# Optimization experiments

Measured on AMD Instinct MI355X. Metric: run time of the kernel, lower is better.

Reference implementation:

```python
import jax, jax.numpy as jnp
import numpy as np

SCALING = 2.0  # alpha / r = 128 / 64


def setup_inputs() -> dict:
    key = jax.random.key(0)
    k1, k2, k3, k4, k5 = jax.random.split(key, 5)
    B, S, DIN, DOUT, R = 4, 2048, 4096, 4096, 64
    x = jax.random.normal(k1, (B, S, DIN), dtype=jnp.float32)
    # int8 quantized weight codes in [-127, 127] (stored as int32 for portability)
    qweight = jax.random.randint(k2, (DOUT, DIN), -127, 128, dtype=jnp.int32)
    # per-output-row absmax dequant scale (already divided by 127)
    scale = jax.random.uniform(k3, (DOUT, 1), dtype=jnp.float32, minval=0.005, maxval=0.02)
    lora_A = jax.random.normal(k4, (R, DIN), dtype=jnp.float32) * 0.02
    lora_B = jax.random.normal(k5, (DOUT, R), dtype=jnp.float32) * 0.02
    return {"x": x, "qweight": qweight, "scale": scale, "lora_A": lora_A, "lora_B": lora_B}


def reference(x, qweight, scale, lora_A, lora_B):
    # inline int8 dequant: w[o,i] = code[o,i] * scale[o]
    w = qweight.astype(x.dtype) * scale  # [DOUT, DIN]
    base = jnp.einsum('bsi,oi->bso', x, w)
    # low-rank LoRA path: (x @ A^T) @ B^T, scaled
    xa = jnp.einsum('bsi,ri->bsr', x, lora_A)       # [B,S,R]
    lora = jnp.einsum('bsr,or->bso', xa, lora_B)    # [B,S,DOUT]
    return base + SCALING * lora
```

## Files before the change

### kernel.cpp

```cpp
#include <hip/hip_runtime.h>
#include <hip/hip_bf16.h>
#include <stdint.h>


typedef __bf16 bf16x8 __attribute__((ext_vector_type(8)));
typedef float f32x4 __attribute__((ext_vector_type(4)));
typedef int i32x4 __attribute__((ext_vector_type(4)));

#define DIN   4096
#define DOUT  4096
#define MTOT  8192
#define RNK   64
#define NT    64

__device__ inline void gload_lds16(const void* g, void* l) {
  __builtin_amdgcn_global_load_lds((const __attribute__((address_space(1))) void*)g,
                                   (__attribute__((address_space(3))) void*)l,
                                   16, 0, 0);
}

__global__ __launch_bounds__(256) void quant_x_kernel(const float* __restrict__ x,
                                                      signed char* __restrict__ Xi8,
                                                      float* __restrict__ tstep) {
  const int row = blockIdx.x, t = threadIdx.x;
  const float4* xr = (const float4*)(x + (size_t)row * DIN);
  float4 v[4];
  float m = 0.f;
#pragma unroll
  for (int s = 0; s < 4; ++s) {
    v[s] = xr[t + s * 256];
    m = fmaxf(m, fmaxf(fmaxf(fabsf(v[s].x), fabsf(v[s].y)),
                       fmaxf(fabsf(v[s].z), fabsf(v[s].w))));
  }
#pragma unroll
  for (int off = 32; off > 0; off >>= 1) m = fmaxf(m, __shfl_xor(m, off));
  __shared__ float wm[4];
  if ((t & 63) == 0) wm[t >> 6] = m;
  __syncthreads();
  m = fmaxf(fmaxf(wm[0], wm[1]), fmaxf(wm[2], wm[3]));
  m = fmaxf(m, 1e-30f);
  const float rs = 127.0f / m;
  int* orow = (int*)(Xi8 + (size_t)row * DIN);
#pragma unroll
  for (int s = 0; s < 4; ++s) {
    float e[4] = {v[s].x, v[s].y, v[s].z, v[s].w};
    union { signed char c[4]; int i; } p;
#pragma unroll
    for (int j = 0; j < 4; ++j) {
      int q = __float2int_rn(e[j] * rs);
      q = q > 127 ? 127 : (q < -127 ? -127 : q);
      p.c[j] = (signed char)q;
    }
    orow[t + s * 256] = p.i;
  }
  if (t == 0) tstep[row] = m * (1.0f / 127.0f);
}

__global__ void cvt_w_kernel(const int* __restrict__ q, signed char* __restrict__ Wi8) {
  int i = blockIdx.x * blockDim.x + threadIdx.x;
  int4 v = ((const int4*)q)[i];
  union { signed char c[4]; int i; } p;
  p.c[0] = (signed char)v.x; p.c[1] = (signed char)v.y;
  p.c[2] = (signed char)v.z; p.c[3] = (signed char)v.w;
  ((int*)Wi8)[i] = p.i;
}

__global__ __launch_bounds__(256) void cvt_ab_kernel(const float* __restrict__ A,
                                                     const float* __restrict__ B,
                                                     signed char* __restrict__ Ai8,
                                                     float* __restrict__ astep,
                                                     __bf16* __restrict__ Blt) {
  const int t = threadIdx.x;
  if (blockIdx.x < 64) {
    const int row = blockIdx.x;
    const float4* ar = (const float4*)(A + (size_t)row * DIN);
    float4 v[4];
    float m = 0.f;
#pragma unroll
    for (int s = 0; s < 4; ++s) {
      v[s] = ar[t + s * 256];
      m = fmaxf(m, fmaxf(fmaxf(fabsf(v[s].x), fabsf(v[s].y)),
                         fmaxf(fabsf(v[s].z), fabsf(v[s].w))));
    }
#pragma unroll
    for (int off = 32; off > 0; off >>= 1) m = fmaxf(m, __shfl_xor(m, off));
    __shared__ float wm[4];
    if ((t & 63) == 0) wm[t >> 6] = m;
    __syncthreads();
    m = fmaxf(fmaxf(wm[0], wm[1]), fmaxf(wm[2], wm[3]));
    m = fmaxf(m, 1e-30f);
    const float rs = 127.0f / m;
    int* orow = (int*)(Ai8 + (size_t)row * DIN);
#pragma unroll
    for (int s = 0; s < 4; ++s) {
      float e[4] = {v[s].x, v[s].y, v[s].z, v[s].w};
      union { signed char c[4]; int i; } p;
#pragma unroll
      for (int j = 0; j < 4; ++j) {
        int q = __float2int_rn(e[j] * rs);
        q = q > 127 ? 127 : (q < -127 ? -127 : q);
        p.c[j] = (signed char)q;
      }
      orow[t + s * 256] = p.i;
    }
    if (t == 0) astep[row] = m * (1.0f / 127.0f);
  } else {
    int i = (blockIdx.x - 64) * 256 + t;
    float4 v = ((const float4*)B)[i];
    union { __bf16 h[4]; uint64_t u; } p;
    p.h[0] = (__bf16)(2.0f * v.x); p.h[1] = (__bf16)(2.0f * v.y);
    p.h[2] = (__bf16)(2.0f * v.z); p.h[3] = (__bf16)(2.0f * v.w);
    ((uint64_t*)Blt)[i] = p.u;
  }
}

__global__ __launch_bounds__(128) void lora_xa_kernel(const signed char* __restrict__ Xi8,
                                                      const float* __restrict__ tstep,
                                                      const signed char* __restrict__ Ai8,
                                                      const float* __restrict__ astep,
                                                      __bf16* __restrict__ xa) {
  int wid = threadIdx.x >> 6, lane = threadIdx.x & 63;
  int rowbase = blockIdx.x * 32 + wid * 16;
  i32x4 acc[4] = {};
  const signed char* xrow = Xi8 + (size_t)(rowbase + (lane & 15)) * DIN + (lane >> 4) * 16;
  const signed char* ab = Ai8 + (size_t)(lane & 15) * DIN + (lane >> 4) * 16;
  for (int k0 = 0; k0 < DIN; k0 += 64) {
    i32x4 af = *(const i32x4*)(xrow + k0);
#pragma unroll
    for (int ni = 0; ni < 4; ++ni) {
      i32x4 bv = *(const i32x4*)(ab + (size_t)ni * 16 * DIN + k0);
      acc[ni] = __builtin_amdgcn_mfma_i32_16x16x64_i8(af, bv, acc[ni], 0, 0, 0);
    }
  }
  f32x4 tm = *(const f32x4*)&tstep[rowbase + (lane >> 4) * 4];
#pragma unroll
  for (int ni = 0; ni < 4; ++ni) {
    const int col = ni * 16 + (lane & 15);
    const float as = astep[col];
#pragma unroll
    for (int j = 0; j < 4; ++j) {
      int row = rowbase + (lane >> 4) * 4 + j;
      xa[(size_t)row * RNK + col] = (__bf16)((float)acc[ni][j] * tm[j] * as);
    }
  }
}

__global__ __launch_bounds__(512, 1) void gemm_i8_kernel(const signed char* __restrict__ Xi8,
                                                         const signed char* __restrict__ Wi8,
                                                         const float* __restrict__ scale,
                                                         const float* __restrict__ tstep,
                                                         const __bf16* __restrict__ xa,
                                                         const __bf16* __restrict__ Blt,
                                                         float* __restrict__ out) {
  extern __shared__ char smem[];
  const int tid = threadIdx.x;
  const int lane = tid & 63;
  const int w = tid >> 6;
  const int wr = w >> 2;
  const int wc = w & 3;

  const int swz = (blockIdx.x & 7) * 64 + (blockIdx.x >> 3);
  const int bx = swz & 15;
  const int by = swz >> 4;
  const size_t bm = (size_t)by * 256, bn = (size_t)bx * 256;

  const int rc = ((lane >> 4) ^ ((lane >> 1) & 3)) << 4;
  const int srow = tid >> 2;
  const int scol = ((tid & 3) ^ ((tid >> 3) & 3)) << 4;

  auto SH = [&](const signed char* g, size_t r0, int srct, int ldsoff) {
    gload_lds16(g + (r0 + srow) * (size_t)4096 + srct * 64 + scol,
                smem + ldsoff + tid * 16);
  };
  auto stage = [&](int srct, int buf) {
    int b = buf * 32768;
    SH(Xi8, bm, srct, b); SH(Xi8, bm + 128, srct, b + 8192);
    SH(Wi8, bn, srct, b + 16384); SH(Wi8, bn + 128, srct, b + 24576);
  };

  i32x4 aP[4], bP[4], aQ[4], bQ[4], a2[4];
  i32x4 acc[8][4] = {};

  stage(0, 0); stage(1, 1); stage(2, 2);
  asm volatile("s_waitcnt vmcnt(4)" ::: "memory");
  __builtin_amdgcn_s_barrier();
  {
    const int ab0 = wr * 8192 + (lane & 15) * 64 + rc;
    const int bb0 = 16384 + (wc >> 1) * 8192 + (wc & 1) * 4096 + (lane & 15) * 64 + rc;
#pragma unroll
    for (int mi = 0; mi < 4; ++mi) aP[mi] = *(const i32x4*)(smem + ab0 + mi * 1024);
#pragma unroll
    for (int ni = 0; ni < 4; ++ni) bP[ni] = *(const i32x4*)(smem + bb0 + ni * 1024);
  }

  auto body = [&](int kt, auto& ac, auto& bc, auto& an, auto& bn) {
    const int bufb = (kt & 3) * 32768;
    const int ab = bufb + wr * 8192 + (lane & 15) * 64 + rc;
    const int bb = bufb + 16384 + (wc >> 1) * 8192 + (wc & 1) * 4096 + (lane & 15) * 64 + rc;
    const int st = (kt + 3 < NT) ? kt + 3 : NT - 1;
    stage(st, (kt + 3) & 3);
#pragma unroll
    for (int mi = 0; mi < 4; ++mi)
      a2[mi] = *(const i32x4*)(smem + ab + 4096 + mi * 1024);
    __builtin_amdgcn_s_setprio(1);
#pragma unroll
    for (int mi = 0; mi < 4; ++mi)
#pragma unroll
      for (int ni = 0; ni < 4; ++ni)
        acc[mi][ni] = __builtin_amdgcn_mfma_i32_16x16x64_i8(ac[mi], bc[ni], acc[mi][ni], 0, 0, 0);
    __builtin_amdgcn_s_setprio(0);
    const int nbufb = ((kt + 1) & 3) * 32768;
    const int nab = nbufb + wr * 8192 + (lane & 15) * 64 + rc;
    const int nbb = nbufb + 16384 + (wc >> 1) * 8192 + (wc & 1) * 4096 + (lane & 15) * 64 + rc;
#pragma unroll
    for (int mi = 0; mi < 4; ++mi) an[mi] = *(const i32x4*)(smem + nab + mi * 1024);
#pragma unroll
    for (int ni = 0; ni < 4; ++ni) bn[ni] = *(const i32x4*)(smem + nbb + ni * 1024);
    __builtin_amdgcn_s_setprio(1);
#pragma unroll
    for (int mi = 0; mi < 4; ++mi)
#pragma unroll
      for (int ni = 0; ni < 4; ++ni)
        acc[4 + mi][ni] = __builtin_amdgcn_mfma_i32_16x16x64_i8(a2[mi], bc[ni], acc[4 + mi][ni], 0, 0, 0);
    __builtin_amdgcn_s_setprio(0);
    __builtin_amdgcn_sched_barrier(0);
    asm volatile("s_waitcnt vmcnt(4)" ::: "memory");
    __builtin_amdgcn_s_barrier();
  };

  for (int kt = 0; kt < NT; kt += 2) {
    body(kt, aP, bP, aQ, bQ);
    body(kt + 1, aQ, bQ, aP, bP);
  }

  const int sl_row = lane >> 3;
  const int sl_col = ((lane & 7) ^ (lane >> 3)) << 4;
  auto SBF = [&](const __bf16* g, size_t r0, int ldsoff) {
    char* d0 = smem + ldsoff + w * 2048 + lane * 16;
#pragma unroll
    for (int s = 0; s < 2; ++s) {
      const int rl = (w * 2 + s) * 8 + sl_row;
      gload_lds16((const char*)g + (r0 + rl) * 128 + sl_col, d0 + s * 1024);
    }
  };
  SBF(xa, bm, 0); SBF(xa, bm + 128, 16384);
  SBF(Blt, bn, 32768); SBF(Blt, bn + 128, 49152);

  float sc[4];
#pragma unroll
  for (int ni = 0; ni < 4; ++ni)
    sc[ni] = scale[bn + wc * 64 + ni * 16 + (lane & 15)];
  f32x4 tm[8];
#pragma unroll
  for (int mi = 0; mi < 8; ++mi)
    tm[mi] = *(const f32x4*)&tstep[bm + wr * 128 + mi * 16 + (lane >> 4) * 4];

  asm volatile("s_waitcnt vmcnt(0)" ::: "memory");
  __builtin_amdgcn_s_barrier();

  const int cx0 = ((lane >> 4) << 4) ^ ((lane & 7) << 4);
  const int cx1 = (64 | ((lane >> 4) << 4)) ^ ((lane & 7) << 4);
  const int abE = wr * 16384 + (lane & 15) * 128;
  const int bbE = 32768 + (wc >> 1) * 16384 + ((wc & 1) * 64 + (lane & 15)) * 128;

  bf16x8 bl0[4], bl1[4];
#pragma unroll
  for (int ni = 0; ni < 4; ++ni) {
    bl0[ni] = *(const bf16x8*)(smem + bbE + ni * 2048 + cx0);
    bl1[ni] = *(const bf16x8*)(smem + bbE + ni * 2048 + cx1);
  }
#pragma unroll
  for (int mi = 0; mi < 8; ++mi) {
    bf16x8 ax0 = *(const bf16x8*)(smem + abE + mi * 2048 + cx0);
    bf16x8 ax1 = *(const bf16x8*)(smem + abE + mi * 2048 + cx1);
    const size_t row = bm + wr * 128 + mi * 16 + (lane >> 4) * 4;
#pragma unroll
    for (int ni = 0; ni < 4; ++ni) {
      f32x4 l = {0.f, 0.f, 0.f, 0.f};
      l = __builtin_amdgcn_mfma_f32_16x16x32_bf16(ax0, bl0[ni], l, 0, 0, 0);
      l = __builtin_amdgcn_mfma_f32_16x16x32_bf16(ax1, bl1[ni], l, 0, 0, 0);
      const size_t col = bn + wc * 64 + ni * 16 + (lane & 15);
#pragma unroll
      for (int j = 0; j < 4; ++j)
        out[(row + j) * DOUT + col] = (float)acc[mi][ni][j] * (sc[ni] * tm[mi][j]) + l[j];
    }
  }
}

extern "C" void kernel_launch(void* const* d_in, const int* in_sizes, int n_in,
                              void* d_out, int out_size, void* d_ws, size_t ws_size,
                              hipStream_t stream) {
  const float* x = (const float*)d_in[0];
  const int* qw = (const int*)d_in[1];
  const float* scale = (const float*)d_in[2];
  const float* lA = (const float*)d_in[3];
  const float* lB = (const float*)d_in[4];
  float* out = (float*)d_out;

  char* ws = (char*)d_ws;
  signed char* Xi8 = (signed char*)ws;
  signed char* Wi8 = (signed char*)(ws + 33554432);
  __bf16* xa    = (__bf16*)(ws + 50331648);
  signed char* Ai8 = (signed char*)(ws + 51380224);
  __bf16* Blt   = (__bf16*)(ws + 51904512);
  float* tstep  = (float*)(ws + 52428800);
  float* astep  = (float*)(ws + 52461568);

  hipFuncSetAttribute((const void*)gemm_i8_kernel,
                      hipFuncAttributeMaxDynamicSharedMemorySize, 131072);

  quant_x_kernel<<<MTOT, 256, 0, stream>>>(x, Xi8, tstep);
  cvt_w_kernel<<<DOUT * (DIN / 4) / 256, 256, 0, stream>>>(qw, Wi8);
  cvt_ab_kernel<<<320, 256, 0, stream>>>(lA, lB, Ai8, astep, Blt);
  lora_xa_kernel<<<MTOT / 32, 128, 0, stream>>>(Xi8, tstep, Ai8, astep, xa);
  gemm_i8_kernel<<<(MTOT / 256) * (DOUT / 256), 512, 131072, stream>>>(
      Xi8, Wi8, scale, tstep, xa, Blt, out);
}
```

Baseline: 212.2 us.

## Merge prep kernels, split LoRA xa reduction over K, drop MFMA setprio

Three preprocessing kernels (x quantization, weight int32-to-int8 conversion, LoRA A/B conversion) are combined into one launch that picks its role from the block index. This removes launch gaps and tail serialization between them. The LoRA x·A^T kernel now splits K across four waves per 16-row block and reduces their results through shared memory, which gives more parallelism and shorter per-wave loops. The s_setprio hints around the main GEMM's MFMA blocks are removed, which changes wave scheduling in the hot loop and could help or hurt.

```diff
diff --git a/kernel.cpp b/kernel.cpp
--- a/kernel.cpp
+++ b/kernel.cpp
@@ -19,66 +19,30 @@
                                    16, 0, 0);
 }
 
-__global__ __launch_bounds__(256) void quant_x_kernel(const float* __restrict__ x,
-                                                      signed char* __restrict__ Xi8,
-                                                      float* __restrict__ tstep) {
-  const int row = blockIdx.x, t = threadIdx.x;
-  const float4* xr = (const float4*)(x + (size_t)row * DIN);
-  float4 v[4];
-  float m = 0.f;
-#pragma unroll
-  for (int s = 0; s < 4; ++s) {
-    v[s] = xr[t + s * 256];
-    m = fmaxf(m, fmaxf(fmaxf(fabsf(v[s].x), fabsf(v[s].y)),
-                       fmaxf(fabsf(v[s].z), fabsf(v[s].w))));
-  }
-#pragma unroll
-  for (int off = 32; off > 0; off >>= 1) m = fmaxf(m, __shfl_xor(m, off));
-  __shared__ float wm[4];
-  if ((t & 63) == 0) wm[t >> 6] = m;
-  __syncthreads();
-  m = fmaxf(fmaxf(wm[0], wm[1]), fmaxf(wm[2], wm[3]));
-  m = fmaxf(m, 1e-30f);
-  const float rs = 127.0f / m;
-  int* orow = (int*)(Xi8 + (size_t)row * DIN);
-#pragma unroll
-  for (int s = 0; s < 4; ++s) {
-    float e[4] = {v[s].x, v[s].y, v[s].z, v[s].w};
-    union { signed char c[4]; int i; } p;
-#pragma unroll
-    for (int j = 0; j < 4; ++j) {
-      int q = __float2int_rn(e[j] * rs);
-      q = q > 127 ? 127 : (q < -127 ? -127 : q);
-      p.c[j] = (signed char)q;
-    }
-    orow[t + s * 256] = p.i;
-  }
-  if (t == 0) tstep[row] = m * (1.0f / 127.0f);
-}
-
-__global__ void cvt_w_kernel(const int* __restrict__ q, signed char* __restrict__ Wi8) {
-  int i = blockIdx.x * blockDim.x + threadIdx.x;
-  int4 v = ((const int4*)q)[i];
-  union { signed char c[4]; int i; } p;
-  p.c[0] = (signed char)v.x; p.c[1] = (signed char)v.y;
-  p.c[2] = (signed char)v.z; p.c[3] = (signed char)v.w;
-  ((int*)Wi8)[i] = p.i;
-}
-
-__global__ __launch_bounds__(256) void cvt_ab_kernel(const float* __restrict__ A,
-                                                     const float* __restrict__ B,
-                                                     signed char* __restrict__ Ai8,
-                                                     float* __restrict__ astep,
-                                                     __bf16* __restrict__ Blt) {
-  const int t = threadIdx.x;
-  if (blockIdx.x < 64) {
-    const int row = blockIdx.x;
-    const float4* ar = (const float4*)(A + (size_t)row * DIN);
+__global__ __launch_bounds__(256) void prep_kernel(const float* __restrict__ x,
+                                                   const int* __restrict__ qw,
+                                                   const float* __restrict__ lA,
+                                                   const float* __restrict__ lB,
+                                                   signed char* __restrict__ Xi8,
+                                                   float* __restrict__ tstep,
+                                                   signed char* __restrict__ Wi8,
+                                                   signed char* __restrict__ Ai8,
+                                                   float* __restrict__ astep,
+                                                   __bf16* __restrict__ Blt) {
+  const int bid = blockIdx.x, t = threadIdx.x;
+  const float* src = nullptr;
+  signed char* dst = nullptr;
+  float* stp = nullptr;
+  int row = 0;
+  if (bid < 8192) { src = x; dst = Xi8; stp = tstep; row = bid; }
+  else if (bid < 8256) { src = lA; dst = Ai8; stp = astep; row = bid - 8192; }
+  if (src) {
+    const float4* xr = (const float4*)(src + (size_t)row * DIN);
     float4 v[4];
     float m = 0.f;
 #pragma unroll
     for (int s = 0; s < 4; ++s) {
-      v[s] = ar[t + s * 256];
+      v[s] = xr[t + s * 256];
       m = fmaxf(m, fmaxf(fmaxf(fabsf(v[s].x), fabsf(v[s].y)),
                          fmaxf(fabsf(v[s].z), fabsf(v[s].w))));
     }
@@ -90,7 +54,7 @@
     m = fmaxf(fmaxf(wm[0], wm[1]), fmaxf(wm[2], wm[3]));
     m = fmaxf(m, 1e-30f);
     const float rs = 127.0f / m;
-    int* orow = (int*)(Ai8 + (size_t)row * DIN);
+    int* orow = (int*)(dst + (size_t)row * DIN);
 #pragma unroll
     for (int s = 0; s < 4; ++s) {
       float e[4] = {v[s].x, v[s].y, v[s].z, v[s].w};
@@ -103,44 +67,62 @@
       }
       orow[t + s * 256] = p.i;
     }
-    if (t == 0) astep[row] = m * (1.0f / 127.0f);
-  } else {
-    int i = (blockIdx.x - 64) * 256 + t;
-    float4 v = ((const float4*)B)[i];
+    if (t == 0) stp[row] = m * (1.0f / 127.0f);
+  } else if (bid < 8512) {
+    int i = (bid - 8256) * 256 + t;
+    float4 v = ((const float4*)lB)[i];
     union { __bf16 h[4]; uint64_t u; } p;
     p.h[0] = (__bf16)(2.0f * v.x); p.h[1] = (__bf16)(2.0f * v.y);
     p.h[2] = (__bf16)(2.0f * v.z); p.h[3] = (__bf16)(2.0f * v.w);
     ((uint64_t*)Blt)[i] = p.u;
-  }
-}
-
-__global__ __launch_bounds__(128) void lora_xa_kernel(const signed char* __restrict__ Xi8,
+  } else {
+    int i = (bid - 8512) * 256 + t;
+    int4 v = ((const int4*)qw)[i];
+    union { signed char c[4]; int i; } p;
+    p.c[0] = (signed char)v.x; p.c[1] = (signed char)v.y;
+    p.c[2] = (signed char)v.z; p.c[3] = (signed char)v.w;
+    ((int*)Wi8)[i] = p.i;
+  }
+}
+
+__global__ __launch_bounds__(256) void lora_xa_kernel(const signed char* __restrict__ Xi8,
                                                       const float* __restrict__ tstep,
                                                       const signed char* __restrict__ Ai8,
                                                       const float* __restrict__ astep,
                                                       __bf16* __restrict__ xa) {
-  int wid = threadIdx.x >> 6, lane = threadIdx.x & 63;
-  int rowbase = blockIdx.x * 32 + wid * 16;
+  __shared__ i32x4 red[4][64][4];
+  const int w = threadIdx.x >> 6, lane = threadIdx.x & 63;
+  const int rowbase = blockIdx.x * 16;
   i32x4 acc[4] = {};
-  const signed char* xrow = Xi8 + (size_t)(rowbase + (lane & 15)) * DIN + (lane >> 4) * 16;
-  const signed char* ab = Ai8 + (size_t)(lane & 15) * DIN + (lane >> 4) * 16;
-  for (int k0 = 0; k0 < DIN; k0 += 64) {
-    i32x4 af = *(const i32x4*)(xrow + k0);
+  const int k00 = w * 1024 + (lane >> 4) * 16;
+  const signed char* xrow = Xi8 + (size_t)(rowbase + (lane & 15)) * DIN + k00;
+  const signed char* ab = Ai8 + (size_t)(lane & 15) * DIN + k00;
+#pragma unroll 4
+  for (int k = 0; k < 1024; k += 64) {
+    i32x4 af = *(const i32x4*)(xrow + k);
 #pragma unroll
     for (int ni = 0; ni < 4; ++ni) {
-      i32x4 bv = *(const i32x4*)(ab + (size_t)ni * 16 * DIN + k0);
+      i32x4 bv = *(const i32x4*)(ab + (size_t)ni * 16 * DIN + k);
       acc[ni] = __builtin_amdgcn_mfma_i32_16x16x64_i8(af, bv, acc[ni], 0, 0, 0);
     }
   }
-  f32x4 tm = *(const f32x4*)&tstep[rowbase + (lane >> 4) * 4];
-#pragma unroll
-  for (int ni = 0; ni < 4; ++ni) {
-    const int col = ni * 16 + (lane & 15);
-    const float as = astep[col];
-#pragma unroll
-    for (int j = 0; j < 4; ++j) {
-      int row = rowbase + (lane >> 4) * 4 + j;
-      xa[(size_t)row * RNK + col] = (__bf16)((float)acc[ni][j] * tm[j] * as);
+#pragma unroll
+  for (int ni = 0; ni < 4; ++ni) red[w][lane][ni] = acc[ni];
+  __syncthreads();
+  if (w == 0) {
+    f32x4 tm = *(const f32x4*)&tstep[rowbase + (lane >> 4) * 4];
+#pragma unroll
+    for (int ni = 0; ni < 4; ++ni) {
+      i32x4 s = red[0][lane][ni];
+#pragma unroll
+      for (int u = 1; u < 4; ++u) s += red[u][lane][ni];
+      const int col = ni * 16 + (lane & 15);
+      const float as = astep[col];
+#pragma unroll
+      for (int j = 0; j < 4; ++j) {
+        int row = rowbase + (lane >> 4) * 4 + j;
+        xa[(size_t)row * RNK + col] = (__bf16)((float)s[j] * tm[j] * as);
+      }
     }
   }
 }
@@ -196,19 +178,16 @@
   auto body = [&](int kt, auto& ac, auto& bc, auto& an, auto& bn) {
     const int bufb = (kt & 3) * 32768;
     const int ab = bufb + wr * 8192 + (lane & 15) * 64 + rc;
-    const int bb = bufb + 16384 + (wc >> 1) * 8192 + (wc & 1) * 4096 + (lane & 15) * 64 + rc;
     const int st = (kt + 3 < NT) ? kt + 3 : NT - 1;
     stage(st, (kt + 3) & 3);
 #pragma unroll
     for (int mi = 0; mi < 4; ++mi)
       a2[mi] = *(const i32x4*)(smem + ab + 4096 + mi * 1024);
-    __builtin_amdgcn_s_setprio(1);
 #pragma unroll
     for (int mi = 0; mi < 4; ++mi)
 #pragma unroll
       for (int ni = 0; ni < 4; ++ni)
         acc[mi][ni] = __builtin_amdgcn_mfma_i32_16x16x64_i8(ac[mi], bc[ni], acc[mi][ni], 0, 0, 0);
-    __builtin_amdgcn_s_setprio(0);
     const int nbufb = ((kt + 1) & 3) * 32768;
     const int nab = nbufb + wr * 8192 + (lane & 15) * 64 + rc;
     const int nbb = nbufb + 16384 + (wc >> 1) * 8192 + (wc & 1) * 4096 + (lane & 15) * 64 + rc;
@@ -216,13 +195,11 @@
     for (int mi = 0; mi < 4; ++mi) an[mi] = *(const i32x4*)(smem + nab + mi * 1024);
 #pragma unroll
     for (int ni = 0; ni < 4; ++ni) bn[ni] = *(const i32x4*)(smem + nbb + ni * 1024);
-    __builtin_amdgcn_s_setprio(1);
 #pragma unroll
     for (int mi = 0; mi < 4; ++mi)
 #pragma unroll
       for (int ni = 0; ni < 4; ++ni)
         acc[4 + mi][ni] = __builtin_amdgcn_mfma_i32_16x16x64_i8(a2[mi], bc[ni], acc[4 + mi][ni], 0, 0, 0);
-    __builtin_amdgcn_s_setprio(0);
     __builtin_amdgcn_sched_barrier(0);
     asm volatile("s_waitcnt vmcnt(4)" ::: "memory");
     __builtin_amdgcn_s_barrier();
@@ -309,10 +286,8 @@
   hipFuncSetAttribute((const void*)gemm_i8_kernel,
                       hipFuncAttributeMaxDynamicSharedMemorySize, 131072);
 
-  quant_x_kernel<<<MTOT, 256, 0, stream>>>(x, Xi8, tstep);
-  cvt_w_kernel<<<DOUT * (DIN / 4) / 256, 256, 0, stream>>>(qw, Wi8);
-  cvt_ab_kernel<<<320, 256, 0, stream>>>(lA, lB, Ai8, astep, Blt);
-  lora_xa_kernel<<<MTOT / 32, 128, 0, stream>>>(Xi8, tstep, Ai8, astep, xa);
+  prep_kernel<<<24896, 256, 0, stream>>>(x, qw, lA, lB, Xi8, tstep, Wi8, Ai8, astep, Blt);
+  lora_xa_kernel<<<MTOT / 16, 256, 0, stream>>>(Xi8, tstep, Ai8, astep, xa);
   gemm_i8_kernel<<<(MTOT / 256) * (DOUT / 256), 512, 131072, stream>>>(
       Xi8, Wi8, scale, tstep, xa, Blt, out);
 }
```

After: 198.9 us (median of 2 runs). 1.07x faster.
